# Performance work log

Hardware: AMD Instinct MI355X
Metric: run time of the kernel (lower is better)

The kernel has to match this reference:

```python
import jax, jax.numpy as jnp
import numpy as np

B, S, NDIMS, NHEADS, NPOS = 1, 2048, 1024, 16, 64
PER_HEAD = NDIMS // NHEADS


def setup_inputs() -> dict:
    key = jax.random.key(0)
    ks = jax.random.split(key, 9)
    sc = 1.0 / np.sqrt(NDIMS)
    inp = {
        'q': jax.random.normal(ks[0], (B, S, NDIMS), jnp.float32),
        'k': jax.random.normal(ks[1], (B, S, NDIMS), jnp.float32),
        'v': jax.random.normal(ks[2], (B, S, NDIMS), jnp.float32),
        'Wq_w': jax.random.normal(ks[3], (NDIMS, NDIMS), jnp.float32) * sc,
        'Wq_b': jnp.zeros((NDIMS,), jnp.float32),
        'Wk_w': jax.random.normal(ks[4], (NDIMS, NDIMS), jnp.float32) * sc,
        'Wk_b': jnp.zeros((NDIMS,), jnp.float32),
        'Wv_w': jax.random.normal(ks[5], (NDIMS, NDIMS), jnp.float32) * sc,
        'Wv_b': jnp.zeros((NDIMS,), jnp.float32),
        'Wo_w': jax.random.normal(ks[6], (NDIMS, NDIMS), jnp.float32) * sc,
        'Wo_b': jnp.zeros((NDIMS,), jnp.float32),
        'pos_emb': jax.random.normal(ks[7], (PER_HEAD, NPOS), jnp.float32) * 0.02,
        'nheads': NHEADS,
    }
    return inp


def cope(query, attn_logits, pos_emb):
    # query: [b,h,q,d]; attn_logits: [b,h,q,k]; pos_emb: [d,npos]
    npos_max = pos_emb.shape[-1]
    gates = jax.nn.sigmoid(attn_logits)
    # reverse cumsum over key axis: flip -> cumsum -> flip
    pos = jnp.flip(jnp.cumsum(jnp.flip(gates, axis=-1), axis=-1), axis=-1)
    pos = jnp.minimum(pos, npos_max - 1)
    pos_ceil = jnp.ceil(pos).astype(jnp.int32)
    pos_floor = jnp.floor(pos).astype(jnp.int32)
    logits_int = jnp.einsum('bhqd,dn->bhqn', query, pos_emb)  # [b,h,q,npos]
    logits_ceil = jnp.take_along_axis(logits_int, pos_ceil, axis=-1)
    logits_floor = jnp.take_along_axis(logits_int, pos_floor, axis=-1)
    w = pos - pos_floor
    return logits_ceil * w + logits_floor * (1.0 - w)


def reference(q, k, v, Wq_w, Wq_b, Wk_w, Wk_b, Wv_w, Wv_b, Wo_w, Wo_b, pos_emb, nheads):
    b, s, ndims = q.shape
    d = ndims // nheads
    def heads(x, W, bb):
        y = x @ W.T + bb
        return y.reshape(b, s, nheads, d).transpose(0, 2, 1, 3)  # [b,h,s,d]
    Q = heads(q, Wq_w, Wq_b)
    K = heads(k, Wk_w, Wk_b)
    V = heads(v, Wv_w, Wv_b)
    logits = jnp.einsum('bhqd,bhkd->bhqk', Q, K) / jnp.sqrt(jnp.asarray(d, Q.dtype))
    scores = jax.nn.softmax(logits + cope(Q, logits, pos_emb), axis=-1)
    out = jnp.einsum('bhqk,bhkd->bhqd', scores, V)
    out = out.transpose(0, 2, 1, 3).reshape(b, s, ndims)
    return out @ Wo_w.T + Wo_b
```

## Files before the change

### kernel.cpp

```cpp
#include <hip/hip_runtime.h>
#include <hip/hip_bf16.h>
#include <math.h>

#define SEQ 2048
#define ND  1024
#define NH  16
#define HD  64
#define NPOSN 64

typedef short short8 __attribute__((ext_vector_type(8)));
typedef short short4v __attribute__((ext_vector_type(4)));
typedef float floatx4 __attribute__((ext_vector_type(4)));

#define MFMA16(A, B, C) __builtin_amdgcn_mfma_f32_16x16x32_bf16((A), (B), (C), 0, 0, 0)

#define ASYNC16(gp, lp)                                                                     \
  __builtin_amdgcn_global_load_lds((const __attribute__((address_space(1))) unsigned int*)(gp), \
                                   (__attribute__((address_space(3))) unsigned int*)(lp), 16, 0, 0)

__device__ __forceinline__ short f2bf(float x) {
  __hip_bfloat16 h = __float2bfloat16(x);
  return *reinterpret_cast<short*>(&h);
}
__device__ __forceinline__ float bf2f(short s) {
  __hip_bfloat16 h = *reinterpret_cast<__hip_bfloat16*>(&s);
  return __bfloat162float(h);
}
__device__ __forceinline__ float lane_bcast(float v, int l) {
  return __int_as_float(__builtin_amdgcn_readlane(__float_as_int(v), l));
}

struct Prep2 {
  const float* x0; short* x0h; short* x0l;
  const float* x1; short* x1h; short* x1l;
  const float* x2; short* x2h; short* x2l;
  const float* w0; short* w0h; short* w0l;
  const float* w1; short* w1h; short* w1l;
  const float* w2; short* w2h; short* w2l;
  const float* w3; short* w3h; short* w3l;
  const float* pe; short* peT;
};

__device__ __forceinline__ void split_planes(const float* __restrict__ in,
                                             short* __restrict__ oh,
                                             short* __restrict__ ol) {
  int r = blockIdx.x;
  int c = threadIdx.x << 2;
  float4 v = *(const float4*)(in + (size_t)r * 1024 + c);
  short4v hi, lo;
  hi.x = f2bf(v.x); lo.x = f2bf(v.x - bf2f(hi.x));
  hi.y = f2bf(v.y); lo.y = f2bf(v.y - bf2f(hi.y));
  hi.z = f2bf(v.z); lo.z = f2bf(v.z - bf2f(hi.z));
  hi.w = f2bf(v.w); lo.w = f2bf(v.w - bf2f(hi.w));
  *(short4v*)(oh + (size_t)r * 1024 + c) = hi;
  *(short4v*)(ol + (size_t)r * 1024 + c) = lo;
}

__global__ __launch_bounds__(256)
void prep2(Prep2 P) {
  const int z = blockIdx.z;
  if (z < 3) {
    const float* in = (z == 0) ? P.x0 : (z == 1 ? P.x1 : P.x2);
    short* oh = (z == 0) ? P.x0h : (z == 1 ? P.x1h : P.x2h);
    short* ol = (z == 0) ? P.x0l : (z == 1 ? P.x1l : P.x2l);
    split_planes(in, oh, ol);
  } else if (z < 7) {
    if (blockIdx.x >= 1024) return;
    const float* in = (z == 3) ? P.w0 : (z == 4 ? P.w1 : (z == 5 ? P.w2 : P.w3));
    short* oh = (z == 3) ? P.w0h : (z == 4 ? P.w1h : (z == 5 ? P.w2h : P.w3h));
    short* ol = (z == 3) ? P.w0l : (z == 4 ? P.w1l : (z == 5 ? P.w2l : P.w3l));
    split_planes(in, oh, ol);
  } else {
    if (blockIdx.x != 0) return;
    for (int i = threadIdx.x; i < 4096; i += 256) {
      int n = i >> 6, d = i & 63;
      P.peT[n * 64 + d] = f2bf(P.pe[d * 64 + n]);
    }
  }
}

struct GArg2 {
  const short* Ahi; const short* Alo;
  const short* Bhi; const short* Blo;
  const float* bias;
  void* o0; void* o1; int mode;
};

__global__ __launch_bounds__(256, 3)
void gemm_planes(GArg2 ga, GArg2 gb, GArg2 gc) {
  __shared__ __align__(16) short Ah[8192];
  __shared__ __align__(16) short Al[8192];
  __shared__ __align__(16) short Bh[4096];
  __shared__ __align__(16) short Bl[4096];
  GArg2 A = (blockIdx.z == 0) ? ga : ((blockIdx.z == 1) ? gb : gc);
  const bool t3 = (A.Blo != nullptr);
  const int t = threadIdx.x;
  const int w = t >> 6, lane = t & 63;
  const int col = lane & 15, quad = lane >> 4;
  const int m0 = blockIdx.x * 128, n0 = blockIdx.y * 64;
  const int wr = (w & 1) * 64, wc = (w >> 1) * 32;
  const int lrow8 = lane >> 3;
  const int src_c = (lane & 7) ^ lrow8;

  floatx4 acc[4][2] = {};
  for (int kk = 0; kk < 1024; kk += 64) {
#pragma unroll
    for (int i = 0; i < 4; ++i) {
      const int inst = 4 * w + i;
      const int row = inst * 8 + lrow8;
      ASYNC16(A.Ahi + (size_t)(m0 + row) * 1024 + kk + src_c * 8, &Ah[inst * 512]);
      ASYNC16(A.Alo + (size_t)(m0 + row) * 1024 + kk + src_c * 8, &Al[inst * 512]);
    }
#pragma unroll
    for (int i = 0; i < 2; ++i) {
      const int inst = 2 * w + i;
      const int row = inst * 8 + lrow8;
      ASYNC16(A.Bhi + (size_t)(n0 + row) * 1024 + kk + src_c * 8, &Bh[inst * 512]);
      if (t3) ASYNC16(A.Blo + (size_t)(n0 + row) * 1024 + kk + src_c * 8, &Bl[inst * 512]);
    }
    __syncthreads();
#pragma unroll
    for (int ks = 0; ks < 2; ++ks) {
      short8 ah[4], al[4], bh[2], bl[2];
#pragma unroll
      for (int mt = 0; mt < 4; ++mt) {
        const int row = wr + mt * 16 + col;
        const int pos = ((ks * 4 + quad) ^ (row & 7)) * 8;
        ah[mt] = *(const short8*)&Ah[row * 64 + pos];
        al[mt] = *(const short8*)&Al[row * 64 + pos];
      }
#pragma unroll
      for (int nt = 0; nt < 2; ++nt) {
        const int row = wc + nt * 16 + col;
        const int pos = ((ks * 4 + quad) ^ (row & 7)) * 8;
        bh[nt] = *(const short8*)&Bh[row * 64 + pos];
        if (t3) bl[nt] = *(const short8*)&Bl[row * 64 + pos];
      }
#pragma unroll
      for (int mt = 0; mt < 4; ++mt)
#pragma unroll
        for (int nt = 0; nt < 2; ++nt) {
          acc[mt][nt] = MFMA16(ah[mt], bh[nt], acc[mt][nt]);
          acc[mt][nt] = MFMA16(al[mt], bh[nt], acc[mt][nt]);
          if (t3) acc[mt][nt] = MFMA16(ah[mt], bl[nt], acc[mt][nt]);
        }
    }
    __syncthreads();
  }
#pragma unroll
  for (int nt = 0; nt < 2; ++nt) {
    const int n = n0 + wc + nt * 16 + col;
    const float bb = A.bias[n];
#pragma unroll
    for (int mt = 0; mt < 4; ++mt)
#pragma unroll
      for (int r = 0; r < 4; ++r) {
        const int m = m0 + wr + mt * 16 + quad * 4 + r;
        const float v = acc[mt][nt][r] + bb;
        if (A.mode == 0) {
          ((float*)A.o0)[(size_t)m * 1024 + n] = v;
        } else {
          const short hi = f2bf(v);
          const int hh = n >> 6, d = n & 63;
          const size_t off = (A.mode == 1) ? ((size_t)(hh * SEQ + m) * 64 + d)
                                           : ((size_t)(hh * 64 + d) * SEQ + m);
          ((short*)A.o0)[off] = hi;
          if (A.o1) {
            const short lo = f2bf(v - bf2f(hi));
            ((short*)A.o1)[off] = lo;
          }
        }
      }
  }
}

__global__ __launch_bounds__(256, 2)
void cope_attn_mfma(const short* __restrict__ Qhi, const short* __restrict__ Qlo,
                    const short* __restrict__ Khi, const short* __restrict__ Vthi,
                    const short* __restrict__ peT,
                    short* __restrict__ AOhi, short* __restrict__ AOlo) {
  __shared__ __align__(16) short Klds[2][4096];
  __shared__ __align__(16) short Vlds[2][4096];
  __shared__ __align__(16) short Phi[4][16][72];
  __shared__ float2 lis2[4][16][65];
  const int tid = threadIdx.x;
  const int w = tid >> 6, lane = tid & 63;
  const int col = lane & 15, quad = lane >> 4;
  const int h = blockIdx.x & 15;
  const int q0 = (blockIdx.x >> 4) * 64 + w * 16;

  const short* Kb = Khi + (size_t)h * SEQ * 64;
  const short* Vb = Vthi + (size_t)h * 64 * SEQ;

  const int lrow8 = lane >> 3;
  const int src_c = (lane & 7) ^ lrow8;

  auto stage = [&](int kt, int buf) {
#pragma unroll
    for (int i = 0; i < 2; ++i) {
      const int inst = 2 * w + i;
      const int row = inst * 8 + lrow8;
      ASYNC16(Kb + (size_t)(kt * 64 + row) * 64 + src_c * 8, &Klds[buf][inst * 512]);
      ASYNC16(Vb + (size_t)row * SEQ + kt * 64 + src_c * 8, &Vlds[buf][inst * 512]);
    }
  };

  short8 qB[2][2];
#pragma unroll
  for (int ks = 0; ks < 2; ++ks) {
    qB[ks][0] = *(const short8*)(Qhi + (size_t)(h * SEQ + q0 + col) * 64 + ks * 32 + quad * 8);
    qB[ks][1] = *(const short8*)(Qlo + (size_t)(h * SEQ + q0 + col) * 64 + ks * 32 + quad * 8);
  }

  stage(31, 0);

  {
    floatx4 li[4] = {};
#pragma unroll
    for (int nt = 0; nt < 4; ++nt)
#pragma unroll
      for (int ks = 0; ks < 2; ++ks) {
        short8 pb = *(const short8*)(peT + (nt * 16 + col) * 64 + ks * 32 + quad * 8);
        li[nt] = MFMA16(qB[ks][0], pb, li[nt]);
        li[nt] = MFMA16(qB[ks][1], pb, li[nt]);
      }
#pragma unroll
    for (int nt = 0; nt < 4; ++nt)
#pragma unroll
      for (int r = 0; r < 4; ++r) {
        const int qr = quad * 4 + r;
        const int pos = nt * 16 + col;
        const float v = li[nt][r];
        lis2[w][qr][pos].x = v;
        if (pos > 0) lis2[w][qr][pos - 1].y = v;
        if (pos == 63) lis2[w][qr][63].y = v;
      }
  }
  __syncthreads();
  const float lis63 = lis2[w][col][63].x;

  float lrow = 0.f;
  float carry = 0.f;
  bool fast = false;
  floatx4 O[4] = {};

  const int swz = col & 7;

#pragma unroll 1
  for (int it = 0; it < 32; ++it) {
    const int kt = 31 - it;
    const int buf = it & 1;
    if (kt > 0) stage(kt - 1, buf ^ 1);

    short8 kf[4][2], vf[2][4];
#pragma unroll
    for (int ksub = 0; ksub < 4; ++ksub)
#pragma unroll
      for (int ks = 0; ks < 2; ++ks)
        kf[ksub][ks] =
            *(const short8*)&Klds[buf][(ksub * 16 + col) * 64 + (((ks * 4 + quad) ^ swz) * 8)];
#pragma unroll
    for (int ks = 0; ks < 2; ++ks)
#pragma unroll
      for (int dt = 0; dt < 4; ++dt)
        vf[ks][dt] =
            *(const short8*)&Vlds[buf][(dt * 16 + col) * 64 + (((ks * 4 + quad) ^ swz) * 8)];

    floatx4 S[4] = {};
#pragma unroll
    for (int ksub = 0; ksub < 4; ++ksub)
#pragma unroll
      for (int ks = 0; ks < 2; ++ks) {
        S[ksub] = MFMA16(kf[ksub][ks], qB[ks][0], S[ksub]);
        S[ksub] = MFMA16(kf[ksub][ks], qB[ks][1], S[ksub]);
      }
    float sv[4][4];
#pragma unroll
    for (int ksub = 0; ksub < 4; ++ksub)
#pragma unroll
      for (int r = 0; r < 4; ++r) sv[ksub][r] = S[ksub][r] * 0.125f;

    if (!fast && __all((int)(carry >= 63.0f))) fast = true;

    float p4[4][4];
    if (fast) {
#pragma unroll
      for (int ksub = 0; ksub < 4; ++ksub)
#pragma unroll
        for (int r = 0; r < 4; ++r) {
          float pr = __expf(sv[ksub][r] + lis63);
          p4[ksub][r] = pr;
          lrow += pr;
        }
    } else {
      float g[4][4];
#pragma unroll
      for (int ksub = 0; ksub < 4; ++ksub)
#pragma unroll
        for (int r = 0; r < 4; ++r)
          g[ksub][r] = __builtin_amdgcn_rcpf(1.0f + __expf(-sv[ksub][r]));
      float l[4][4], S4[4];
#pragma unroll
      for (int ksub = 0; ksub < 4; ++ksub) {
        l[ksub][3] = g[ksub][3];
        l[ksub][2] = l[ksub][3] + g[ksub][2];
        l[ksub][1] = l[ksub][2] + g[ksub][1];
        l[ksub][0] = l[ksub][1] + g[ksub][0];
        S4[ksub] = l[ksub][0];
      }
      float Sq[4], T[4];
#pragma unroll
      for (int ksub = 0; ksub < 4; ++ksub) {
        float d16 = __shfl_down(S4[ksub], 16, 64);
        float d32 = __shfl_down(S4[ksub], 32, 64);
        float d48 = __shfl_down(S4[ksub], 48, 64);
        float u16 = __shfl_up(S4[ksub], 16, 64);
        float u32 = __shfl_up(S4[ksub], 32, 64);
        float u48 = __shfl_up(S4[ksub], 48, 64);
        float sq = ((quad < 3) ? d16 : 0.f) + ((quad < 2) ? d32 : 0.f) + ((quad < 1) ? d48 : 0.f);
        float pq = ((quad > 0) ? u16 : 0.f) + ((quad > 1) ? u32 : 0.f) + ((quad > 2) ? u48 : 0.f);
        Sq[ksub] = sq;
        T[ksub] = pq + S4[ksub] + sq;
      }
      float U[4];
      U[3] = carry;
      U[2] = U[3] + T[3];
      U[1] = U[2] + T[2];
      U[0] = U[1] + T[1];
      carry = U[0] + T[0];
#pragma unroll
      for (int ksub = 0; ksub < 4; ++ksub)
#pragma unroll
        for (int r = 0; r < 4; ++r) {
          float p = fminf(U[ksub] + Sq[ksub] + l[ksub][r], 63.0f);
          float pf = floorf(p);
          int fi = (int)pf;
          float wq = p - pf;
          float2 lfc = lis2[w][col][fi];
          float pr = __expf(sv[ksub][r] + lfc.x + wq * (lfc.y - lfc.x));
          p4[ksub][r] = pr;
          lrow += pr;
        }
    }
#pragma unroll
    for (int ksub = 0; ksub < 4; ++ksub)
#pragma unroll
      for (int rp = 0; rp < 2; ++rp) {
        short h0 = f2bf(p4[ksub][2 * rp]);
        short h1 = f2bf(p4[ksub][2 * rp + 1]);
        *(int*)&Phi[w][col][ksub * 16 + quad * 4 + 2 * rp] =
            (unsigned short)h0 | ((unsigned)(unsigned short)h1 << 16);
      }
    short8 pa[2];
#pragma unroll
    for (int ks = 0; ks < 2; ++ks)
      pa[ks] = *(const short8*)&Phi[w][col][ks * 32 + quad * 8];
#pragma unroll
    for (int ks = 0; ks < 2; ++ks)
#pragma unroll
      for (int dt = 0; dt < 4; ++dt)
        O[dt] = MFMA16(pa[ks], vf[ks][dt], O[dt]);

    __syncthreads();
  }

  float lr = lrow;
  lr += __shfl_xor(lr, 16, 64);
  lr += __shfl_xor(lr, 32, 64);
  float inv[4];
#pragma unroll
  for (int r = 0; r < 4; ++r) inv[r] = 1.0f / __shfl(lr, quad * 4 + r, 64);
#pragma unroll
  for (int dt = 0; dt < 4; ++dt)
#pragma unroll
    for (int r = 0; r < 4; ++r) {
      float val = O[dt][r] * inv[r];
      int q = q0 + quad * 4 + r;
      int cg = h * 64 + dt * 16 + col;
      short hi = f2bf(val), lo = f2bf(val - bf2f(hi));
      AOhi[(size_t)q * 1024 + cg] = hi;
      AOlo[(size_t)q * 1024 + cg] = lo;
    }
}

template <int MODE>
__global__ __launch_bounds__(256)
void gemm_bt_f32(const float* __restrict__ X, const float* __restrict__ W,
                 const float* __restrict__ bias, float* __restrict__ C,
                 int M, int N, int K) {
  __shared__ __align__(16) float Xs[16][68];
  __shared__ __align__(16) float Ws[16][68];
  const int t = threadIdx.x;
  const int tx = t & 15, ty = t >> 4;
  const int m0 = blockIdx.x * 64, n0 = blockIdx.y * 64;
  const int r = t >> 2;
  const int c4 = (t & 3) << 2;
  const float* Xp = X + (size_t)(m0 + r) * K + c4;
  const float* Wp = W + (size_t)(n0 + r) * K + c4;
  float acc[4][4] = {};
  for (int k0 = 0; k0 < K; k0 += 16) {
    float4 xv = *(const float4*)(Xp + k0);
    float4 wv = *(const float4*)(Wp + k0);
    __syncthreads();
    Xs[c4 + 0][r] = xv.x; Xs[c4 + 1][r] = xv.y; Xs[c4 + 2][r] = xv.z; Xs[c4 + 3][r] = xv.w;
    Ws[c4 + 0][r] = wv.x; Ws[c4 + 1][r] = wv.y; Ws[c4 + 2][r] = wv.z; Ws[c4 + 3][r] = wv.w;
    __syncthreads();
#pragma unroll
    for (int k = 0; k < 16; ++k) {
      const float4 xr = *(const float4*)&Xs[k][ty << 2];
      const float4 wr = *(const float4*)&Ws[k][tx << 2];
      const float xa[4] = {xr.x, xr.y, xr.z, xr.w};
      const float wa[4] = {wr.x, wr.y, wr.z, wr.w};
#pragma unroll
      for (int i = 0; i < 4; ++i)
#pragma unroll
        for (int j = 0; j < 4; ++j) acc[i][j] += xa[i] * wa[j];
    }
  }
#pragma unroll
  for (int i = 0; i < 4; ++i) {
    const int m = m0 + (ty << 2) + i;
#pragma unroll
    for (int j = 0; j < 4; ++j) {
      const int n = n0 + (tx << 2) + j;
      const float v = acc[i][j] + bias[n];
      if (MODE == 0) C[(size_t)m * N + n] = v;
      else { const int hh = n >> 6, d = n & 63; C[((size_t)hh * SEQ + m) * HD + d] = v; }
    }
  }
}

__global__ __launch_bounds__(256)
void cope_attn_f32(const float* __restrict__ Qh, const float* __restrict__ Kh,
                   const float* __restrict__ Vh, const float* __restrict__ pe,
                   float* __restrict__ AO) {
  __shared__ float Kt[64][65];
  __shared__ float Vt[64][65];
  __shared__ float lis[16][64];
  const int t = threadIdx.x;
  const int lane = t & 63;
  const int w = t >> 6;
  const int h = blockIdx.y;
  const int qbase = blockIdx.x * 16 + w * 4;
  float qreg[4];
#pragma unroll
  for (int rr = 0; rr < 4; ++rr)
    qreg[rr] = Qh[((size_t)h * SEQ + qbase + rr) * HD + lane];
  float li[4] = {0.f, 0.f, 0.f, 0.f};
  for (int d = 0; d < 64; ++d) {
    const float pv = pe[d * NPOSN + lane];
#pragma unroll
    for (int rr = 0; rr < 4; ++rr) li[rr] += lane_bcast(qreg[rr], d) * pv;
  }
#pragma unroll
  for (int rr = 0; rr < 4; ++rr) lis[w * 4 + rr][lane] = li[rr];
  float mrow[4] = {-1e30f, -1e30f, -1e30f, -1e30f};
  float lrow[4] = {0.f, 0.f, 0.f, 0.f};
  float carry[4] = {0.f, 0.f, 0.f, 0.f};
  float acc[4] = {0.f, 0.f, 0.f, 0.f};
  for (int kt = (SEQ / 64) - 1; kt >= 0; --kt) {
    const int k0 = kt * 64;
    __syncthreads();
#pragma unroll
    for (int i = 0; i < 4; ++i) {
      const int lin = t + i * 256;
      const int row = lin >> 4, cc = (lin & 15) << 2;
      const float4 kv = *(const float4*)(Kh + ((size_t)h * SEQ + k0 + row) * HD + cc);
      Kt[row][cc + 0] = kv.x; Kt[row][cc + 1] = kv.y; Kt[row][cc + 2] = kv.z; Kt[row][cc + 3] = kv.w;
      const float4 vv = *(const float4*)(Vh + ((size_t)h * SEQ + k0 + row) * HD + cc);
      Vt[row][cc + 0] = vv.x; Vt[row][cc + 1] = vv.y; Vt[row][cc + 2] = vv.z; Vt[row][cc + 3] = vv.w;
    }
    __syncthreads();
    float svv[4] = {0.f, 0.f, 0.f, 0.f};
#pragma unroll
    for (int d = 0; d < 64; ++d) {
      const float kd = Kt[lane][d];
#pragma unroll
      for (int rr = 0; rr < 4; ++rr) svv[rr] += lane_bcast(qreg[rr], d) * kd;
    }
    float p4[4], scl[4];
#pragma unroll
    for (int rr = 0; rr < 4; ++rr) {
      const float s = svv[rr] * 0.125f;
      const float gg = 1.0f / (1.0f + __expf(-s));
      float gs = gg;
#pragma unroll
      for (int off = 1; off < 64; off <<= 1) {
        const float tt = __shfl_down(gs, off, 64);
        gs += (lane + off < 64) ? tt : 0.0f;
      }
      const float tot = lane_bcast(gs, 0);
      float p = carry[rr] + gs;
      carry[rr] += tot;
      p = fminf(p, 63.0f);
      const float pf = floorf(p);
      const float wq = p - pf;
      const int fi = (int)pf;
      const int ci = (int)ceilf(p);
      const float cope = lis[w * 4 + rr][ci] * wq + lis[w * 4 + rr][fi] * (1.0f - wq);
      const float av = s + cope;
      float mt = av;
#pragma unroll
      for (int off = 32; off > 0; off >>= 1) mt = fmaxf(mt, __shfl_xor(mt, off, 64));
      const float nm = fmaxf(mrow[rr], mt);
      const float sc = __expf(mrow[rr] - nm);
      const float p2 = __expf(av - nm);
      float psum = p2;
#pragma unroll
      for (int off = 32; off > 0; off >>= 1) psum += __shfl_xor(psum, off, 64);
      lrow[rr] = lrow[rr] * sc + psum;
      mrow[rr] = nm;
      p4[rr] = p2;
      scl[rr] = sc;
    }
#pragma unroll
    for (int rr = 0; rr < 4; ++rr) acc[rr] *= scl[rr];
#pragma unroll
    for (int j = 0; j < 64; ++j) {
      const float vj = Vt[j][lane];
#pragma unroll
      for (int rr = 0; rr < 4; ++rr) acc[rr] += lane_bcast(p4[rr], j) * vj;
    }
  }
#pragma unroll
  for (int rr = 0; rr < 4; ++rr)
    AO[(size_t)(qbase + rr) * ND + h * HD + lane] = acc[rr] / lrow[rr];
}

extern "C" void kernel_launch(void* const* d_in, const int* in_sizes, int n_in,
                              void* d_out, int out_size, void* d_ws, size_t ws_size,
                              hipStream_t stream) {
  (void)in_sizes; (void)n_in; (void)out_size;
  const float* q    = (const float*)d_in[0];
  const float* k    = (const float*)d_in[1];
  const float* v    = (const float*)d_in[2];
  const float* Wq_w = (const float*)d_in[3];
  const float* Wq_b = (const float*)d_in[4];
  const float* Wk_w = (const float*)d_in[5];
  const float* Wk_b = (const float*)d_in[6];
  const float* Wv_w = (const float*)d_in[7];
  const float* Wv_b = (const float*)d_in[8];
  const float* Wo_w = (const float*)d_in[9];
  const float* Wo_b = (const float*)d_in[10];
  const float* pe   = (const float*)d_in[11];
  float* out = (float*)d_out;
  char* ws = (char*)d_ws;

  const size_t XP = (size_t)SEQ * 1024 * 2;
  const size_t WP = (size_t)1024 * 1024 * 2;
  const size_t HB = (size_t)SEQ * 1024 * 2;
  const size_t NEED = 6 * XP + 8 * WP + 4 * HB + 8192;

  if (ws_size >= NEED) {
    short* Xqh = (short*)ws;               short* Xql = (short*)(ws + XP);
    short* Xkh = (short*)(ws + 2 * XP);    short* Xkl = (short*)(ws + 3 * XP);
    short* Xvh = (short*)(ws + 4 * XP);    short* Xvl = (short*)(ws + 5 * XP);
    char*  wb  = ws + 6 * XP;
    short* Wqh = (short*)wb;               short* Wql = (short*)(wb + WP);
    short* Wkh = (short*)(wb + 2 * WP);    short* Wkl = (short*)(wb + 3 * WP);
    short* Wvh = (short*)(wb + 4 * WP);    short* Wvl = (short*)(wb + 5 * WP);
    short* Woh = (short*)(wb + 6 * WP);    short* Wol = (short*)(wb + 7 * WP);
    char*  hb  = wb + 8 * WP;
    short* Qhi = (short*)hb;               short* Qlo = (short*)(hb + HB);
    short* Khi = (short*)(hb + 2 * HB);    short* Vthi = (short*)(hb + 3 * HB);
    short* peT = (short*)(hb + 4 * HB);
    short* AOhi = Xqh;
    short* AOlo = Xql;

    Prep2 P{q, Xqh, Xql, k, Xkh, Xkl, v, Xvh, Xvl,
            Wq_w, Wqh, Wql, Wk_w, Wkh, Wkl, Wv_w, Wvh, Wvl, Wo_w, Woh, Wol,
            pe, peT};
    prep2<<<dim3(2048, 1, 8), 256, 0, stream>>>(P);
    GArg2 aq{Xqh, Xql, Wqh, Wql, Wq_b, Qhi, Qlo, 1};
    GArg2 ak{Xkh, Xkl, Wkh, nullptr, Wk_b, Khi, nullptr, 1};
    GArg2 av{Xvh, Xvl, Wvh, nullptr, Wv_b, Vthi, nullptr, 2};
    gemm_planes<<<dim3(16, 16, 3), 256, 0, stream>>>(aq, ak, av);
    cope_attn_mfma<<<512, 256, 0, stream>>>(Qhi, Qlo, Khi, Vthi, peT, AOhi, AOlo);
    GArg2 ao{AOhi, AOlo, Woh, Wol, Wo_b, (void*)out, nullptr, 0};
    gemm_planes<<<dim3(16, 16, 1), 256, 0, stream>>>(ao, ao, ao);
  } else {
    const size_t per = (size_t)NH * SEQ * HD;
    float* Qh = (float*)d_ws;
    float* Kh = Qh + per;
    float* Vh = Kh + per;
    float* AO = Vh + per;
    dim3 gblk(256), ggrd(SEQ / 64, ND / 64);
    gemm_bt_f32<1><<<ggrd, gblk, 0, stream>>>(q, Wq_w, Wq_b, Qh, SEQ, ND, ND);
    gemm_bt_f32<1><<<ggrd, gblk, 0, stream>>>(k, Wk_w, Wk_b, Kh, SEQ, ND, ND);
    gemm_bt_f32<1><<<ggrd, gblk, 0, stream>>>(v, Wv_w, Wv_b, Vh, SEQ, ND, ND);
    cope_attn_f32<<<dim3(SEQ / 16, NH), 256, 0, stream>>>(Qh, Kh, Vh, pe, AO);
    gemm_bt_f32<0><<<ggrd, gblk, 0, stream>>>(AO, Wo_w, Wo_b, out, SEQ, ND, ND);
  }
}
```

Before: 209.1 us.

## Double-buffer GEMM K-loop and software-pipeline PV MFMA in CoPE attention

The projection GEMM now uses two 32-wide K tiles in LDS instead of one 64-wide tile. The next tile is prefetched while the current one is computed, which removes one barrier per iteration. In the attention kernel, the P·V MFMA for iteration i runs during iteration i+1, after the QK MFMAs, using a double-buffered, swizzled P tile and V fragments held in registers. This is meant to overlap the softmax and CoPE scalar work with matrix ops. The CoPE interpolation table is also packed as bf16 pairs in one int to shrink LDS, which costs some precision in the position logits.

```diff
diff --git a/kernel.cpp b/kernel.cpp
--- a/kernel.cpp
+++ b/kernel.cpp
@@ -88,10 +88,10 @@
 
 __global__ __launch_bounds__(256, 3)
 void gemm_planes(GArg2 ga, GArg2 gb, GArg2 gc) {
-  __shared__ __align__(16) short Ah[8192];
-  __shared__ __align__(16) short Al[8192];
-  __shared__ __align__(16) short Bh[4096];
-  __shared__ __align__(16) short Bl[4096];
+  __shared__ __align__(16) short Ah[2][4096];
+  __shared__ __align__(16) short Al[2][4096];
+  __shared__ __align__(16) short Bh[2][2048];
+  __shared__ __align__(16) short Bl[2][2048];
   GArg2 A = (blockIdx.z == 0) ? ga : ((blockIdx.z == 1) ? gb : gc);
   const bool t3 = (A.Blo != nullptr);
   const int t = threadIdx.x;
@@ -99,53 +99,55 @@
   const int col = lane & 15, quad = lane >> 4;
   const int m0 = blockIdx.x * 128, n0 = blockIdx.y * 64;
   const int wr = (w & 1) * 64, wc = (w >> 1) * 32;
-  const int lrow8 = lane >> 3;
-  const int src_c = (lane & 7) ^ lrow8;
-
-  floatx4 acc[4][2] = {};
-  for (int kk = 0; kk < 1024; kk += 64) {
-#pragma unroll
-    for (int i = 0; i < 4; ++i) {
-      const int inst = 4 * w + i;
-      const int row = inst * 8 + lrow8;
-      ASYNC16(A.Ahi + (size_t)(m0 + row) * 1024 + kk + src_c * 8, &Ah[inst * 512]);
-      ASYNC16(A.Alo + (size_t)(m0 + row) * 1024 + kk + src_c * 8, &Al[inst * 512]);
-    }
+  const int r16 = lane >> 2;
+  const int chnk = (lane & 3) ^ (r16 & 3);
+
+  auto stage = [&](int k, int buf) {
+    const int kk = k * 32;
 #pragma unroll
     for (int i = 0; i < 2; ++i) {
       const int inst = 2 * w + i;
-      const int row = inst * 8 + lrow8;
-      ASYNC16(A.Bhi + (size_t)(n0 + row) * 1024 + kk + src_c * 8, &Bh[inst * 512]);
-      if (t3) ASYNC16(A.Blo + (size_t)(n0 + row) * 1024 + kk + src_c * 8, &Bl[inst * 512]);
-    }
+      const int row = inst * 16 + r16;
+      ASYNC16(A.Ahi + (size_t)(m0 + row) * 1024 + kk + chnk * 8, &Ah[buf][inst * 512]);
+      ASYNC16(A.Alo + (size_t)(m0 + row) * 1024 + kk + chnk * 8, &Al[buf][inst * 512]);
+    }
+    {
+      const int row = w * 16 + r16;
+      ASYNC16(A.Bhi + (size_t)(n0 + row) * 1024 + kk + chnk * 8, &Bh[buf][w * 512]);
+      if (t3) ASYNC16(A.Blo + (size_t)(n0 + row) * 1024 + kk + chnk * 8, &Bl[buf][w * 512]);
+    }
+  };
+
+  floatx4 acc[4][2] = {};
+  stage(0, 0);
+#pragma unroll 1
+  for (int it = 0; it < 32; ++it) {
+    const int buf = it & 1;
     __syncthreads();
-#pragma unroll
-    for (int ks = 0; ks < 2; ++ks) {
-      short8 ah[4], al[4], bh[2], bl[2];
-#pragma unroll
-      for (int mt = 0; mt < 4; ++mt) {
-        const int row = wr + mt * 16 + col;
-        const int pos = ((ks * 4 + quad) ^ (row & 7)) * 8;
-        ah[mt] = *(const short8*)&Ah[row * 64 + pos];
-        al[mt] = *(const short8*)&Al[row * 64 + pos];
-      }
+    if (it < 31) stage(it + 1, buf ^ 1);
+    short8 ah[4], al[4], bh[2], bl[2];
+#pragma unroll
+    for (int mt = 0; mt < 4; ++mt) {
+      const int row = wr + mt * 16 + col;
+      const int pos = (quad ^ (row & 3)) * 8;
+      ah[mt] = *(const short8*)&Ah[buf][row * 32 + pos];
+      al[mt] = *(const short8*)&Al[buf][row * 32 + pos];
+    }
+#pragma unroll
+    for (int nt = 0; nt < 2; ++nt) {
+      const int row = wc + nt * 16 + col;
+      const int pos = (quad ^ (row & 3)) * 8;
+      bh[nt] = *(const short8*)&Bh[buf][row * 32 + pos];
+      if (t3) bl[nt] = *(const short8*)&Bl[buf][row * 32 + pos];
+    }
+#pragma unroll
+    for (int mt = 0; mt < 4; ++mt)
 #pragma unroll
       for (int nt = 0; nt < 2; ++nt) {
-        const int row = wc + nt * 16 + col;
-        const int pos = ((ks * 4 + quad) ^ (row & 7)) * 8;
-        bh[nt] = *(const short8*)&Bh[row * 64 + pos];
-        if (t3) bl[nt] = *(const short8*)&Bl[row * 64 + pos];
-      }
-#pragma unroll
-      for (int mt = 0; mt < 4; ++mt)
-#pragma unroll
-        for (int nt = 0; nt < 2; ++nt) {
-          acc[mt][nt] = MFMA16(ah[mt], bh[nt], acc[mt][nt]);
-          acc[mt][nt] = MFMA16(al[mt], bh[nt], acc[mt][nt]);
-          if (t3) acc[mt][nt] = MFMA16(ah[mt], bl[nt], acc[mt][nt]);
-        }
-    }
-    __syncthreads();
+        acc[mt][nt] = MFMA16(ah[mt], bh[nt], acc[mt][nt]);
+        acc[mt][nt] = MFMA16(al[mt], bh[nt], acc[mt][nt]);
+        if (t3) acc[mt][nt] = MFMA16(ah[mt], bl[nt], acc[mt][nt]);
+      }
   }
 #pragma unroll
   for (int nt = 0; nt < 2; ++nt) {
@@ -181,8 +183,9 @@
                     short* __restrict__ AOhi, short* __restrict__ AOlo) {
   __shared__ __align__(16) short Klds[2][4096];
   __shared__ __align__(16) short Vlds[2][4096];
-  __shared__ __align__(16) short Phi[4][16][72];
-  __shared__ float2 lis2[4][16][65];
+  __shared__ __align__(16) short Phi[2][4][16][64];
+  __shared__ int lisP[4][16][64];
+  __shared__ float lis63s[4][16];
   const int tid = threadIdx.x;
   const int w = tid >> 6, lane = tid & 63;
   const int col = lane & 15, quad = lane >> 4;
@@ -194,6 +197,7 @@
 
   const int lrow8 = lane >> 3;
   const int src_c = (lane & 7) ^ lrow8;
+  const int swz = col & 7;
 
   auto stage = [&](int kt, int buf) {
 #pragma unroll
@@ -231,40 +235,36 @@
         const int qr = quad * 4 + r;
         const int pos = nt * 16 + col;
         const float v = li[nt][r];
-        lis2[w][qr][pos].x = v;
-        if (pos > 0) lis2[w][qr][pos - 1].y = v;
-        if (pos == 63) lis2[w][qr][63].y = v;
+        const short bv = f2bf(v);
+        short* sp = (short*)&lisP[w][qr][0];
+        sp[2 * pos] = bv;
+        if (pos > 0) sp[2 * pos - 1] = bv;
+        if (pos == 63) { sp[127] = bv; lis63s[w][qr] = v; }
       }
   }
   __syncthreads();
-  const float lis63 = lis2[w][col][63].x;
+  const float lis63 = lis63s[w][col];
 
   float lrow = 0.f;
   float carry = 0.f;
   bool fast = false;
   floatx4 O[4] = {};
-
-  const int swz = col & 7;
+  short8 vfs[2][4];
 
 #pragma unroll 1
   for (int it = 0; it < 32; ++it) {
     const int kt = 31 - it;
     const int buf = it & 1;
+    const int pb = it & 1;
     if (kt > 0) stage(kt - 1, buf ^ 1);
 
-    short8 kf[4][2], vf[2][4];
+    short8 kf[4][2];
 #pragma unroll
     for (int ksub = 0; ksub < 4; ++ksub)
 #pragma unroll
       for (int ks = 0; ks < 2; ++ks)
         kf[ksub][ks] =
             *(const short8*)&Klds[buf][(ksub * 16 + col) * 64 + (((ks * 4 + quad) ^ swz) * 8)];
-#pragma unroll
-    for (int ks = 0; ks < 2; ++ks)
-#pragma unroll
-      for (int dt = 0; dt < 4; ++dt)
-        vf[ks][dt] =
-            *(const short8*)&Vlds[buf][(dt * 16 + col) * 64 + (((ks * 4 + quad) ^ swz) * 8)];
 
     floatx4 S[4] = {};
 #pragma unroll
@@ -274,6 +274,19 @@
         S[ksub] = MFMA16(kf[ksub][ks], qB[ks][0], S[ksub]);
         S[ksub] = MFMA16(kf[ksub][ks], qB[ks][1], S[ksub]);
       }
+
+    if (it > 0) {
+      short8 pa[2];
+#pragma unroll
+      for (int ks = 0; ks < 2; ++ks)
+        pa[ks] = *(const short8*)&Phi[pb ^ 1][w][col][((ks * 4 + quad) ^ swz) * 8];
+#pragma unroll
+      for (int ks = 0; ks < 2; ++ks)
+#pragma unroll
+        for (int dt = 0; dt < 4; ++dt)
+          O[dt] = MFMA16(pa[ks], vfs[ks][dt], O[dt]);
+    }
+
     float sv[4][4];
 #pragma unroll
     for (int ksub = 0; ksub < 4; ++ksub)
@@ -336,32 +349,47 @@
           float pf = floorf(p);
           int fi = (int)pf;
           float wq = p - pf;
-          float2 lfc = lis2[w][col][fi];
-          float pr = __expf(sv[ksub][r] + lfc.x + wq * (lfc.y - lfc.x));
+          int pp = lisP[w][col][fi];
+          float lf = bf2f((short)(pp & 0xffff));
+          float lc = bf2f((short)((unsigned)pp >> 16));
+          float pr = __expf(sv[ksub][r] + lf + wq * (lc - lf));
           p4[ksub][r] = pr;
           lrow += pr;
         }
     }
+
 #pragma unroll
     for (int ksub = 0; ksub < 4; ++ksub)
 #pragma unroll
       for (int rp = 0; rp < 2; ++rp) {
         short h0 = f2bf(p4[ksub][2 * rp]);
         short h1 = f2bf(p4[ksub][2 * rp + 1]);
-        *(int*)&Phi[w][col][ksub * 16 + quad * 4 + 2 * rp] =
+        const int posi = ksub * 16 + quad * 4 + 2 * rp;
+        const int addr = (((posi >> 3) ^ swz) << 3) + (posi & 7);
+        *(int*)&Phi[pb][w][col][addr] =
             (unsigned short)h0 | ((unsigned)(unsigned short)h1 << 16);
       }
+
+#pragma unroll
+    for (int ks = 0; ks < 2; ++ks)
+#pragma unroll
+      for (int dt = 0; dt < 4; ++dt)
+        vfs[ks][dt] =
+            *(const short8*)&Vlds[buf][(dt * 16 + col) * 64 + (((ks * 4 + quad) ^ swz) * 8)];
+
+    __syncthreads();
+  }
+
+  {
     short8 pa[2];
 #pragma unroll
     for (int ks = 0; ks < 2; ++ks)
-      pa[ks] = *(const short8*)&Phi[w][col][ks * 32 + quad * 8];
+      pa[ks] = *(const short8*)&Phi[1][w][col][((ks * 4 + quad) ^ swz) * 8];
 #pragma unroll
     for (int ks = 0; ks < 2; ++ks)
 #pragma unroll
       for (int dt = 0; dt < 4; ++dt)
-        O[dt] = MFMA16(pa[ks], vf[ks][dt], O[dt]);
-
-    __syncthreads();
+        O[dt] = MFMA16(pa[ks], vfs[ks][dt], O[dt]);
   }
 
   float lr = lrow;
```

New measurement: 238.2 us. 1.14x slower.
